# Performance work log

Measured on AMD Instinct MI355X. Metric: run time of the kernel, lower is better.

Reference implementation:

```python
import jax, jax.numpy as jnp
import numpy as np

B, D, H, O, E = 1048576, 17, 8, 6, 4  # batch, input_dim, expert_hidden, output_dim, n_clusters
G1, G2 = 64, 32  # gating hidden dims


def setup_inputs() -> dict:
    key = jax.random.key(0)
    ks = jax.random.split(key, 14)
    def w(k, shape, fan_in):
        return (jax.random.normal(k, shape, jnp.float32) / jnp.sqrt(jnp.float32(fan_in)))
    return {
        "x": jax.random.normal(ks[0], (B, D), jnp.float32),
        # per-expert MLP params, stacked on leading expert axis E
        "eW1": w(ks[1], (E, D, H), D), "eb1": w(ks[2], (E, H), D),
        "eW2": w(ks[3], (E, H, H), H), "eb2": w(ks[4], (E, H), H),
        "eW3": w(ks[5], (E, H, O), H), "eb3": w(ks[6], (E, O), H),
        # gating classifier params
        "gW1": w(ks[7], (D, G1), D), "gb1": w(ks[8], (G1,), D),
        "gW2": w(ks[9], (G1, G2), G1), "gb2": w(ks[10], (G2,), G1),
        "gW3": w(ks[11], (G2, E), G2), "gb3": w(ks[12], (E,), G2),
    }


def reference(x, eW1, eb1, eW2, eb2, eW3, eb3, gW1, gb1, gW2, gb2, gW3, gb3):
    # gating network: 17 -> 64 -> 32 -> 4 logits
    h = jax.nn.relu(x @ gW1 + gb1)
    h = jax.nn.relu(h @ gW2 + gb2)
    gating_logits = h @ gW3 + gb3  # [B, E]
    selected = jnp.argmax(gating_logits, axis=1)  # [B] hard routing
    # all experts computed (as in the original), stacked over expert axis
    e = jax.nn.relu(jnp.einsum('bi,eih->beh', x, eW1) + eb1)   # [B, E, H]
    e = jax.nn.relu(jnp.einsum('beh,ehk->bek', e, eW2) + eb2)  # [B, E, H]
    eo = jnp.einsum('bek,eko->beo', e, eW3) + eb3              # [B, E, O]
    # gather the selected expert's output per sample
    predictions = jnp.take_along_axis(eo, selected[:, None, None], axis=1)[:, 0, :]  # [B, O]
    return predictions, gating_logits
```

## Files before the change

### kernel.cpp

```cpp
#include <hip/hip_runtime.h>

#define BTOT 1048576
#define D 17
#define H 8
#define OUT 6
#define E 4
#define G1 64
#define G2 32

__global__ __launch_bounds__(256) void hybrid_ruc_kernel(
    const float* __restrict__ x,
    const float* __restrict__ eW1, const float* __restrict__ eb1,
    const float* __restrict__ eW2, const float* __restrict__ eb2,
    const float* __restrict__ eW3, const float* __restrict__ eb3,
    const float* __restrict__ gW1, const float* __restrict__ gb1,
    const float* __restrict__ gW2, const float* __restrict__ gb2,
    const float* __restrict__ gW3, const float* __restrict__ gb3,
    float* __restrict__ out)
{
    __shared__ float sx[256 * D];
    const int tid = threadIdx.x;
    const long long bbase = (long long)blockIdx.x * 256;

    #pragma unroll
    for (int k = 0; k < D; ++k) {
        int t = tid + k * 256;
        sx[t] = x[bbase * D + t];
    }
    __syncthreads();

    float xr[D];
    #pragma unroll
    for (int i = 0; i < D; ++i) xr[i] = sx[tid * D + i];

    float h2[G2];
    #pragma unroll
    for (int j = 0; j < G2; ++j) h2[j] = gb2[j];

    #pragma unroll 1
    for (int jt = 0; jt < G1 / 16; ++jt) {
        float h1t[16];
        #pragma unroll
        for (int c = 0; c < 16; ++c) h1t[c] = gb1[jt * 16 + c];
        #pragma unroll
        for (int i = 0; i < D; ++i) {
            const float xi = xr[i];
            const float* w1row = gW1 + i * G1 + jt * 16;
            #pragma unroll
            for (int c = 0; c < 16; ++c)
                h1t[c] = __builtin_fmaf(xi, w1row[c], h1t[c]);
        }
        #pragma unroll
        for (int c = 0; c < 16; ++c) {
            const float hv = fmaxf(h1t[c], 0.0f);
            const float* w2row = gW2 + (jt * 16 + c) * G2;
            #pragma unroll
            for (int j = 0; j < G2; ++j)
                h2[j] = __builtin_fmaf(hv, w2row[j], h2[j]);
        }
    }

    float lg[E];
    #pragma unroll
    for (int e = 0; e < E; ++e) lg[e] = gb3[e];
    #pragma unroll
    for (int j = 0; j < G2; ++j) {
        const float hv = fmaxf(h2[j], 0.0f);
        #pragma unroll
        for (int e = 0; e < E; ++e)
            lg[e] = __builtin_fmaf(hv, gW3[j * E + e], lg[e]);
    }

    int sel = 0;
    float best = lg[0];
    #pragma unroll
    for (int e = 1; e < E; ++e) {
        if (lg[e] > best) { best = lg[e]; sel = e; }
    }

    float pred[OUT];
    #pragma unroll
    for (int o = 0; o < OUT; ++o) pred[o] = 0.0f;

    #pragma unroll 1
    for (int e = 0; e < E; ++e) {
        float t1[H];
        #pragma unroll
        for (int h = 0; h < H; ++h) t1[h] = eb1[e * H + h];
        #pragma unroll
        for (int i = 0; i < D; ++i) {
            const float xi = xr[i];
            const float* w = eW1 + e * D * H + i * H;
            #pragma unroll
            for (int h = 0; h < H; ++h)
                t1[h] = __builtin_fmaf(xi, w[h], t1[h]);
        }
        float t2[H];
        #pragma unroll
        for (int h = 0; h < H; ++h) t2[h] = eb2[e * H + h];
        #pragma unroll
        for (int k = 0; k < H; ++k) {
            const float tv = fmaxf(t1[k], 0.0f);
            const float* w = eW2 + e * H * H + k * H;
            #pragma unroll
            for (int h = 0; h < H; ++h)
                t2[h] = __builtin_fmaf(tv, w[h], t2[h]);
        }
        float po[OUT];
        #pragma unroll
        for (int o = 0; o < OUT; ++o) po[o] = eb3[e * OUT + o];
        #pragma unroll
        for (int k = 0; k < H; ++k) {
            const float tv = fmaxf(t2[k], 0.0f);
            const float* w = eW3 + e * H * OUT + k * OUT;
            #pragma unroll
            for (int o = 0; o < OUT; ++o)
                po[o] = __builtin_fmaf(tv, w[o], po[o]);
        }
        #pragma unroll
        for (int o = 0; o < OUT; ++o)
            pred[o] = (sel == e) ? po[o] : pred[o];
    }

    const long long b = bbase + tid;
    #pragma unroll
    for (int o = 0; o < OUT; ++o) out[b * OUT + o] = pred[o];
    float* lout = out + (long long)BTOT * OUT;
    #pragma unroll
    for (int e = 0; e < E; ++e) lout[b * E + e] = lg[e];
}

extern "C" void kernel_launch(void* const* d_in, const int* in_sizes, int n_in,
                              void* d_out, int out_size, void* d_ws, size_t ws_size,
                              hipStream_t stream) {
    const float* x   = (const float*)d_in[0];
    const float* eW1 = (const float*)d_in[1];
    const float* eb1 = (const float*)d_in[2];
    const float* eW2 = (const float*)d_in[3];
    const float* eb2 = (const float*)d_in[4];
    const float* eW3 = (const float*)d_in[5];
    const float* eb3 = (const float*)d_in[6];
    const float* gW1 = (const float*)d_in[7];
    const float* gb1 = (const float*)d_in[8];
    const float* gW2 = (const float*)d_in[9];
    const float* gb2 = (const float*)d_in[10];
    const float* gW3 = (const float*)d_in[11];
    const float* gb3 = (const float*)d_in[12];
    float* out = (float*)d_out;

    dim3 grid(BTOT / 256), block(256);
    hipLaunchKernelGGL(hybrid_ruc_kernel, grid, block, 0, stream,
                       x, eW1, eb1, eW2, eb2, eW3, eb3,
                       gW1, gb1, gW2, gb2, gW3, gb3, out);
}
```

Before: 217.6 us.

## Rewrite gating and expert MLPs with bf16 MFMA using split-precision emulation

Replaces the scalar FP32 FMA kernel with a two-kernel design. A tiny pre-kernel converts the weights into bf16 tiles, split into three precision levels for the gating network. The main kernel runs the gating layers on 16x16x32 bf16 MFMA with a 3-way split that emulates FP32 accuracy, and runs the expert layers in plain bf16 MFMA, masking the non-selected experts in layer 2. Per-wave LDS staging, swizzled layouts and vectorized stores are added. Expert outputs computed in single bf16 may lose precision relative to the FP32 reference, and the extra launch adds a small fixed cost.

```diff
diff --git a/kernel.cpp b/kernel.cpp
--- a/kernel.cpp
+++ b/kernel.cpp
@@ -8,126 +8,311 @@
 #define G1 64
 #define G2 32
 
-__global__ __launch_bounds__(256) void hybrid_ruc_kernel(
+typedef short bf8 __attribute__((ext_vector_type(8)));
+typedef float f4 __attribute__((ext_vector_type(4), aligned(16)));
+typedef float f4u __attribute__((ext_vector_type(4), aligned(4)));
+typedef float f2u __attribute__((ext_vector_type(2), aligned(4)));
+typedef unsigned int u4 __attribute__((ext_vector_type(4)));
+
+#define MFMA16 __builtin_amdgcn_mfma_f32_16x16x32_bf16
+
+__device__ __forceinline__ unsigned int fbits(float x){ union{float f; unsigned int u;} a; a.f = x; return a.u; }
+__device__ __forceinline__ float bitsf(unsigned int u){ union{unsigned int u; float f;} a; a.u = u; return a.f; }
+__device__ __forceinline__ unsigned short bf_rne(float x){ unsigned int u = fbits(x); u += 0x7FFFu + ((u>>16)&1u); return (unsigned short)(u>>16); }
+
+__device__ __forceinline__ void split2(float a, float b,
+                                       unsigned int& q1, unsigned int& q2, unsigned int& q3){
+    unsigned int ua = fbits(a), ub = fbits(b);
+    unsigned int a1 = ua & 0xFFFF0000u, b1 = ub & 0xFFFF0000u;
+    float ra = a - bitsf(a1), rb = b - bitsf(b1);
+    unsigned int a2 = fbits(ra) & 0xFFFF0000u, b2 = fbits(rb) & 0xFFFF0000u;
+    float ra2 = ra - bitsf(a2), rb2 = rb - bitsf(b2);
+    unsigned int a3 = fbits(ra2); a3 += 0x7FFFu + ((a3>>16)&1u);
+    unsigned int b3 = fbits(rb2); b3 += 0x7FFFu + ((b3>>16)&1u);
+    q1 = b1 | (a1 >> 16);
+    q2 = b2 | (a2 >> 16);
+    q3 = (b3 & 0xFFFF0000u) | (a3 >> 16);
+}
+
+__device__ __forceinline__ void split8(f4 lo, f4 hi, bf8& A1, bf8& A2, bf8& A3){
+    unsigned int p1[4], p2[4], p3[4];
+    split2(lo.x, lo.y, p1[0], p2[0], p3[0]);
+    split2(lo.z, lo.w, p1[1], p2[1], p3[1]);
+    split2(hi.x, hi.y, p1[2], p2[2], p3[2]);
+    split2(hi.z, hi.w, p1[3], p2[3], p3[3]);
+    union { u4 u; bf8 s; } r1, r2, r3;
+    r1.u = (u4){p1[0], p1[1], p1[2], p1[3]};
+    r2.u = (u4){p2[0], p2[1], p2[2], p2[3]};
+    r3.u = (u4){p3[0], p3[1], p3[2], p3[3]};
+    A1 = r1.s; A2 = r2.s; A3 = r3.s;
+}
+
+__device__ __forceinline__ unsigned short split_level(float w, int l){
+    unsigned int u1 = fbits(w) & 0xFFFF0000u;
+    if (l == 0) return (unsigned short)(u1 >> 16);
+    float r = w - bitsf(u1);
+    unsigned int u2 = fbits(r) & 0xFFFF0000u;
+    if (l == 1) return (unsigned short)(u2 >> 16);
+    float r2 = r - bitsf(u2);
+    return bf_rne(r2);
+}
+
+__global__ void hybrid_pre(const float* __restrict__ eW1, const float* __restrict__ eW2,
+                           const float* __restrict__ eW3, const float* __restrict__ gW1,
+                           const float* __restrict__ gW2, unsigned short* __restrict__ wsB)
+{
+    const int t = threadIdx.x;
+    for (int i = t; i < 3*64*32; i += 256) {
+        int k = i & 31, n = (i >> 5) & 63, l = i >> 11;
+        float w = (k < D) ? gW1[k*G1 + n] : 0.f;
+        wsB[i] = split_level(w, l);
+    }
+    for (int i = t; i < 3*32*64; i += 256) {
+        int k = i & 63, n = (i >> 6) & 31, l = i >> 11;
+        float w = gW2[k*G2 + n];
+        wsB[6144 + i] = split_level(w, l);
+    }
+    for (int i = t; i < 1024; i += 256) {
+        int k = i & 31, n = i >> 5, e = n >> 3, h = n & 7;
+        float w = (k < D) ? eW1[(e*D + k)*H + h] : 0.f;
+        wsB[12288 + i] = bf_rne(w);
+    }
+    for (int i = t; i < 1024; i += 256) {
+        int k = i & 31, n = i >> 5, e = n >> 3, j = n & 7, kk = k - e*8;
+        float w = (kk >= 0 && kk < 8) ? eW2[(e*H + kk)*H + j] : 0.f;
+        wsB[13312 + i] = bf_rne(w);
+    }
+    for (int i = t; i < 512; i += 256) {
+        int k = i & 31, n = i >> 5, e = k >> 3, kk = k & 7;
+        float w = (n < OUT) ? eW3[(e*H + kk)*OUT + n] : 0.f;
+        wsB[14336 + i] = bf_rne(w);
+    }
+}
+
+__global__ __launch_bounds__(256, 2) void hybrid_main(
     const float* __restrict__ x,
-    const float* __restrict__ eW1, const float* __restrict__ eb1,
-    const float* __restrict__ eW2, const float* __restrict__ eb2,
-    const float* __restrict__ eW3, const float* __restrict__ eb3,
-    const float* __restrict__ gW1, const float* __restrict__ gb1,
-    const float* __restrict__ gW2, const float* __restrict__ gb2,
+    const float* __restrict__ eb1, const float* __restrict__ eb2, const float* __restrict__ eb3,
+    const float* __restrict__ gb1, const float* __restrict__ gb2,
     const float* __restrict__ gW3, const float* __restrict__ gb3,
+    const unsigned short* __restrict__ wsB,
     float* __restrict__ out)
 {
-    __shared__ float sx[256 * D];
+    __shared__ char lds_all[4 * 16384];
     const int tid = threadIdx.x;
-    const long long bbase = (long long)blockIdx.x * 256;
-
-    #pragma unroll
-    for (int k = 0; k < D; ++k) {
-        int t = tid + k * 256;
-        sx[t] = x[bbase * D + t];
-    }
-    __syncthreads();
-
-    float xr[D];
-    #pragma unroll
-    for (int i = 0; i < D; ++i) xr[i] = sx[tid * D + i];
-
-    float h2[G2];
-    #pragma unroll
-    for (int j = 0; j < G2; ++j) h2[j] = gb2[j];
-
-    #pragma unroll 1
-    for (int jt = 0; jt < G1 / 16; ++jt) {
-        float h1t[16];
-        #pragma unroll
-        for (int c = 0; c < 16; ++c) h1t[c] = gb1[jt * 16 + c];
-        #pragma unroll
-        for (int i = 0; i < D; ++i) {
-            const float xi = xr[i];
-            const float* w1row = gW1 + i * G1 + jt * 16;
-            #pragma unroll
-            for (int c = 0; c < 16; ++c)
-                h1t[c] = __builtin_fmaf(xi, w1row[c], h1t[c]);
-        }
-        #pragma unroll
-        for (int c = 0; c < 16; ++c) {
-            const float hv = fmaxf(h1t[c], 0.0f);
-            const float* w2row = gW2 + (jt * 16 + c) * G2;
-            #pragma unroll
-            for (int j = 0; j < G2; ++j)
-                h2[j] = __builtin_fmaf(hv, w2row[j], h2[j]);
-        }
-    }
-
-    float lg[E];
-    #pragma unroll
-    for (int e = 0; e < E; ++e) lg[e] = gb3[e];
-    #pragma unroll
-    for (int j = 0; j < G2; ++j) {
-        const float hv = fmaxf(h2[j], 0.0f);
-        #pragma unroll
-        for (int e = 0; e < E; ++e)
-            lg[e] = __builtin_fmaf(hv, gW3[j * E + e], lg[e]);
-    }
-
-    int sel = 0;
-    float best = lg[0];
-    #pragma unroll
-    for (int e = 1; e < E; ++e) {
-        if (lg[e] > best) { best = lg[e]; sel = e; }
-    }
-
-    float pred[OUT];
-    #pragma unroll
-    for (int o = 0; o < OUT; ++o) pred[o] = 0.0f;
-
-    #pragma unroll 1
-    for (int e = 0; e < E; ++e) {
-        float t1[H];
-        #pragma unroll
-        for (int h = 0; h < H; ++h) t1[h] = eb1[e * H + h];
-        #pragma unroll
-        for (int i = 0; i < D; ++i) {
-            const float xi = xr[i];
-            const float* w = eW1 + e * D * H + i * H;
-            #pragma unroll
-            for (int h = 0; h < H; ++h)
-                t1[h] = __builtin_fmaf(xi, w[h], t1[h]);
-        }
-        float t2[H];
-        #pragma unroll
-        for (int h = 0; h < H; ++h) t2[h] = eb2[e * H + h];
-        #pragma unroll
-        for (int k = 0; k < H; ++k) {
-            const float tv = fmaxf(t1[k], 0.0f);
-            const float* w = eW2 + e * H * H + k * H;
-            #pragma unroll
-            for (int h = 0; h < H; ++h)
-                t2[h] = __builtin_fmaf(tv, w[h], t2[h]);
-        }
-        float po[OUT];
-        #pragma unroll
-        for (int o = 0; o < OUT; ++o) po[o] = eb3[e * OUT + o];
-        #pragma unroll
-        for (int k = 0; k < H; ++k) {
-            const float tv = fmaxf(t2[k], 0.0f);
-            const float* w = eW3 + e * H * OUT + k * OUT;
-            #pragma unroll
-            for (int o = 0; o < OUT; ++o)
-                po[o] = __builtin_fmaf(tv, w[o], po[o]);
-        }
-        #pragma unroll
-        for (int o = 0; o < OUT; ++o)
-            pred[o] = (sel == e) ? po[o] : pred[o];
-    }
-
-    const long long b = bbase + tid;
-    #pragma unroll
-    for (int o = 0; o < OUT; ++o) out[b * OUT + o] = pred[o];
-    float* lout = out + (long long)BTOT * OUT;
-    #pragma unroll
-    for (int e = 0; e < E; ++e) lout[b * E + e] = lg[e];
+    const int wave = tid >> 6, lane = tid & 63;
+    const int q = lane >> 4, c = lane & 15;
+    char* slice = lds_all + wave * 16384;
+    float* sx   = (float*)slice;
+    float* sh1  = (float*)slice;
+    float* sh2  = (float*)slice;
+    unsigned short* sAe2 = (unsigned short*)slice;
+    unsigned short* sAe3 = (unsigned short*)(slice + 5120);
+    float* spred = (float*)(slice + 10240);
+    int*   ssel  = (int*)(slice + 12288);
+
+    const long long samp0 = (long long)blockIdx.x * 256 + wave * 64;
+
+    {
+        const float* xr = x + (samp0 + lane) * D;
+        f4u x0 = *(const f4u*)xr, x1 = *(const f4u*)(xr+4);
+        f4u x2 = *(const f4u*)(xr+8), x3 = *(const f4u*)(xr+12);
+        float x16 = xr[16];
+        float* dst = sx + lane * 36;
+        *(f4*)(dst)      = (f4){x0.x,x0.y,x0.z,x0.w};
+        *(f4*)(dst + 4)  = (f4){x1.x,x1.y,x1.z,x1.w};
+        *(f4*)(dst + 8)  = (f4){x2.x,x2.y,x2.z,x2.w};
+        *(f4*)(dst + 12) = (f4){x3.x,x3.y,x3.z,x3.w};
+        *(f4*)(dst + 16) = (f4){x16, 0.f, 0.f, 0.f};
+        *(f4*)(dst + 20) = (f4){0.f,0.f,0.f,0.f};
+        *(f4*)(dst + 24) = (f4){0.f,0.f,0.f,0.f};
+        *(f4*)(dst + 28) = (f4){0.f,0.f,0.f,0.f};
+    }
+    __builtin_amdgcn_wave_barrier();
+
+    bf8 B1f[4][3];
+    #pragma unroll
+    for (int nt = 0; nt < 4; ++nt)
+        #pragma unroll
+        for (int l = 0; l < 3; ++l)
+            B1f[nt][l] = *(const bf8*)(wsB + ((l*64 + nt*16 + c)*32 + q*8));
+    float bias1[4];
+    #pragma unroll
+    for (int nt = 0; nt < 4; ++nt) bias1[nt] = gb1[nt*16 + c];
+
+    bf8 A1[4], A2[4], A3[4];
+    #pragma unroll
+    for (int mt = 0; mt < 4; ++mt) {
+        const float* src = sx + (mt*16 + c)*36 + q*8;
+        f4 lo = *(const f4*)src, hi = *(const f4*)(src + 4);
+        split8(lo, hi, A1[mt], A2[mt], A3[mt]);
+    }
+    __builtin_amdgcn_wave_barrier();
+
+    #pragma unroll
+    for (int mt = 0; mt < 4; ++mt) {
+        #pragma unroll
+        for (int nt = 0; nt < 4; ++nt) {
+            f4 am = {0.f,0.f,0.f,0.f}, ac = {0.f,0.f,0.f,0.f};
+            am = MFMA16(A1[mt], B1f[nt][0], am, 0,0,0);
+            ac = MFMA16(A1[mt], B1f[nt][1], ac, 0,0,0);
+            ac = MFMA16(A2[mt], B1f[nt][0], ac, 0,0,0);
+            ac = MFMA16(A1[mt], B1f[nt][2], ac, 0,0,0);
+            ac = MFMA16(A2[mt], B1f[nt][1], ac, 0,0,0);
+            ac = MFMA16(A3[mt], B1f[nt][0], ac, 0,0,0);
+            ac = MFMA16(A3[mt], B1f[nt][1], ac, 0,0,0);
+            #pragma unroll
+            for (int r = 0; r < 4; ++r) {
+                float h = fmaxf(am[r] + ac[r] + bias1[nt], 0.f);
+                int row = mt*16 + q*4 + r;
+                int blk = (nt*2 + (c>>3)) ^ (row & 7);
+                sh1[row*64 + blk*8 + (c&7)] = h;
+            }
+        }
+    }
+    __builtin_amdgcn_wave_barrier();
+
+    bf8 B2f[2][2][3];
+    #pragma unroll
+    for (int nt = 0; nt < 2; ++nt)
+        #pragma unroll
+        for (int ks = 0; ks < 2; ++ks)
+            #pragma unroll
+            for (int l = 0; l < 3; ++l)
+                B2f[nt][ks][l] = *(const bf8*)(wsB + 6144 + ((l*32 + nt*16 + c)*64 + ks*32 + q*8));
+    float bias2[2];
+    #pragma unroll
+    for (int nt = 0; nt < 2; ++nt) bias2[nt] = gb2[nt*16 + c];
+
+    #pragma unroll
+    for (int mt = 0; mt < 4; ++mt) {
+        bf8 C1[2], C2[2], C3[2];
+        #pragma unroll
+        for (int ks = 0; ks < 2; ++ks) {
+            int row = mt*16 + c;
+            int blk = (ks*4 + q) ^ (row & 7);
+            const float* src = sh1 + row*64 + blk*8;
+            f4 lo = *(const f4*)src, hi = *(const f4*)(src + 4);
+            split8(lo, hi, C1[ks], C2[ks], C3[ks]);
+        }
+        #pragma unroll
+        for (int nt = 0; nt < 2; ++nt) {
+            f4 am = {0.f,0.f,0.f,0.f}, ac = {0.f,0.f,0.f,0.f};
+            #pragma unroll
+            for (int ks = 0; ks < 2; ++ks) {
+                am = MFMA16(C1[ks], B2f[nt][ks][0], am, 0,0,0);
+                ac = MFMA16(C1[ks], B2f[nt][ks][1], ac, 0,0,0);
+                ac = MFMA16(C2[ks], B2f[nt][ks][0], ac, 0,0,0);
+                ac = MFMA16(C1[ks], B2f[nt][ks][2], ac, 0,0,0);
+                ac = MFMA16(C2[ks], B2f[nt][ks][1], ac, 0,0,0);
+                ac = MFMA16(C3[ks], B2f[nt][ks][0], ac, 0,0,0);
+                ac = MFMA16(C3[ks], B2f[nt][ks][1], ac, 0,0,0);
+            }
+            #pragma unroll
+            for (int r = 0; r < 4; ++r) {
+                float h = fmaxf(am[r] + ac[r] + bias2[nt], 0.f);
+                int row = mt*16 + q*4 + r;
+                sh2[row*36 + nt*16 + c] = h;
+            }
+        }
+    }
+    __builtin_amdgcn_wave_barrier();
+
+    {
+        const float* hr = sh2 + lane*36;
+        f4 hv[8];
+        #pragma unroll
+        for (int i = 0; i < 8; ++i) hv[i] = *(const f4*)(hr + i*4);
+        float lg[E];
+        #pragma unroll
+        for (int e = 0; e < E; ++e) lg[e] = gb3[e];
+        #pragma unroll
+        for (int k = 0; k < G2; ++k) {
+            float h = hv[k>>2][k&3];
+            #pragma unroll
+            for (int e = 0; e < E; ++e)
+                lg[e] = __builtin_fmaf(h, gW3[k*E + e], lg[e]);
+        }
+        int sel = 0; float best = lg[0];
+        #pragma unroll
+        for (int e = 1; e < E; ++e) if (lg[e] > best) { best = lg[e]; sel = e; }
+        ssel[lane] = sel;
+        float* lo = out + (long long)BTOT * OUT + (samp0 + lane) * E;
+        *(f4*)lo = (f4){lg[0], lg[1], lg[2], lg[3]};
+    }
+    __builtin_amdgcn_wave_barrier();
+
+    bf8 Be1f[2], Be2f[2], Be3f;
+    #pragma unroll
+    for (int nt = 0; nt < 2; ++nt) {
+        Be1f[nt] = *(const bf8*)(wsB + 12288 + (nt*16 + c)*32 + q*8);
+        Be2f[nt] = *(const bf8*)(wsB + 13312 + (nt*16 + c)*32 + q*8);
+    }
+    Be3f = *(const bf8*)(wsB + 14336 + c*32 + q*8);
+    float be1v[2], be2v[2];
+    #pragma unroll
+    for (int nt = 0; nt < 2; ++nt) { be1v[nt] = eb1[nt*16 + c]; be2v[nt] = eb2[nt*16 + c]; }
+
+    #pragma unroll
+    for (int mt = 0; mt < 4; ++mt) {
+        #pragma unroll
+        for (int nt = 0; nt < 2; ++nt) {
+            f4 acc = {0.f,0.f,0.f,0.f};
+            acc = MFMA16(A1[mt], Be1f[nt], acc, 0,0,0);
+            #pragma unroll
+            for (int r = 0; r < 4; ++r) {
+                float t = fmaxf(acc[r] + be1v[nt], 0.f);
+                int row = mt*16 + q*4 + r;
+                sAe2[row*40 + nt*16 + c] = (unsigned short)(fbits(t) >> 16);
+            }
+        }
+    }
+    __builtin_amdgcn_wave_barrier();
+
+    #pragma unroll
+    for (int mt = 0; mt < 4; ++mt) {
+        bf8 Af = *(const bf8*)(sAe2 + (mt*16 + c)*40 + q*8);
+        f4 acc[2];
+        #pragma unroll
+        for (int nt = 0; nt < 2; ++nt) {
+            acc[nt] = (f4){0.f,0.f,0.f,0.f};
+            acc[nt] = MFMA16(Af, Be2f[nt], acc[nt], 0,0,0);
+        }
+        #pragma unroll
+        for (int r = 0; r < 4; ++r) {
+            int row = mt*16 + q*4 + r;
+            int se = ssel[row];
+            #pragma unroll
+            for (int nt = 0; nt < 2; ++nt) {
+                int ecol = nt*2 + (c>>3);
+                float t = (se == ecol) ? fmaxf(acc[nt][r] + be2v[nt], 0.f) : 0.f;
+                sAe3[row*40 + nt*16 + c] = (unsigned short)(fbits(t) >> 16);
+            }
+        }
+    }
+    __builtin_amdgcn_wave_barrier();
+
+    #pragma unroll
+    for (int mt = 0; mt < 4; ++mt) {
+        bf8 Af = *(const bf8*)(sAe3 + (mt*16 + c)*40 + q*8);
+        f4 acc = {0.f,0.f,0.f,0.f};
+        acc = MFMA16(Af, Be3f, acc, 0,0,0);
+        #pragma unroll
+        for (int r = 0; r < 4; ++r) {
+            int row = mt*16 + q*4 + r;
+            int se = ssel[row];
+            if (c < OUT) spred[row*8 + c] = acc[r] + eb3[se*OUT + c];
+        }
+    }
+    __builtin_amdgcn_wave_barrier();
+
+    {
+        const float* pr = spred + lane*8;
+        f4 p0 = *(const f4*)pr;
+        float p4 = pr[4], p5 = pr[5];
+        float* po = out + (samp0 + lane) * OUT;
+        *(f4u*)po = p0;
+        *(f2u*)(po + 4) = (f2u){p4, p5};
+    }
 }
 
 extern "C" void kernel_launch(void* const* d_in, const int* in_sizes, int n_in,
@@ -147,9 +332,10 @@
     const float* gW3 = (const float*)d_in[11];
     const float* gb3 = (const float*)d_in[12];
     float* out = (float*)d_out;
-
-    dim3 grid(BTOT / 256), block(256);
-    hipLaunchKernelGGL(hybrid_ruc_kernel, grid, block, 0, stream,
-                       x, eW1, eb1, eW2, eb2, eW3, eb3,
-                       gW1, gb1, gW2, gb2, gW3, gb3, out);
-}
+    unsigned short* wsB = (unsigned short*)d_ws;
+
+    hipLaunchKernelGGL(hybrid_pre, dim3(1), dim3(256), 0, stream,
+                       eW1, eW2, eW3, gW1, gW2, wsB);
+    hipLaunchKernelGGL(hybrid_main, dim3(BTOT / 256), dim3(256), 0, stream,
+                       x, eb1, eb2, eb3, gb1, gb2, gW3, gb3, wsB, out);
+}
```

Result: no change. 220.2 us (+1.2%).
